# Kernel optimization log

Hardware: AMD Instinct MI355X
Metric: run time of the kernel (lower is better)

The kernel has to match this reference:

```python
import jax, jax.numpy as jnp
import numpy as np

L_RTN = 3  # complex taps produced by the RTN head (w_rtn3 out dim = 2*L_RTN)
EPS = 1e-12


def _to_complex(x):
    # (B, 2n) real interleaved [re0, im0, re1, im1, ...] -> (B, n) complex
    return x[:, 0::2] + 1j * x[:, 1::2]


def _to_real(xc):
    # (B, n) complex -> (B, 2n) real interleaved
    b, n = xc.shape
    return jnp.stack([xc.real, xc.imag], axis=-1).reshape(b, 2 * n)


def _complex_conv_taps(h_c, x_c):
    # per-sample causal complex FIR: out[t] = sum_l h[l] * x[t-l]
    # h_c: (B, L) complex, x_c: (B, n) complex
    n = x_c.shape[1]
    out = jnp.zeros_like(x_c)
    for l in range(h_c.shape[1]):  # L is tiny and static
        shifted = jnp.pad(x_c, ((0, 0), (l, 0)))[:, :n]
        out = out + h_c[:, l:l + 1] * shifted
    return out


def setup_inputs() -> dict:
    key = jax.random.key(0)
    ks = jax.random.split(key, 16)
    B, D_IN, H1, CH, H_RTN, H2, D_OUT = 8192, 512, 4096, 256, 1024, 4096, 512
    s = 0.02  # weight init scale
    x = jax.random.normal(ks[0], (B, D_IN), jnp.float32)
    w1 = s * jax.random.normal(ks[1], (H1, D_IN), jnp.float32)
    b1 = jnp.zeros((H1,), jnp.float32)
    w2 = s * jax.random.normal(ks[2], (CH, H1), jnp.float32)
    b2 = jnp.zeros((CH,), jnp.float32)
    w_rtn1 = s * jax.random.normal(ks[3], (H_RTN, CH), jnp.float32)
    b_rtn1 = jnp.zeros((H_RTN,), jnp.float32)
    w_rtn2 = s * jax.random.normal(ks[4], (H_RTN, H_RTN), jnp.float32)
    b_rtn2 = jnp.zeros((H_RTN,), jnp.float32)
    w_rtn3 = s * jax.random.normal(ks[5], (2 * L_RTN, H_RTN), jnp.float32)
    # bias so that RTN starts near identity tap [1, 0, 0, ...]
    b_rtn3 = jnp.zeros((2 * L_RTN,), jnp.float32).at[0].set(1.0)
    w3 = s * jax.random.normal(ks[6], (H2, CH), jnp.float32)
    b3 = jnp.zeros((H2,), jnp.float32)
    w4 = s * jax.random.normal(ks[7], (D_OUT, H2), jnp.float32)
    b4 = jnp.zeros((D_OUT,), jnp.float32)
    h = jax.random.normal(ks[8], (2,), jnp.float32)
    h = h / jnp.linalg.norm(h)  # unit-power single-tap fading channel
    noise = 0.1 * jax.random.normal(ks[9], (B, CH), jnp.float32)
    return {"x": x, "w1": w1, "b1": b1, "w2": w2, "b2": b2,
            "w_rtn1": w_rtn1, "b_rtn1": b_rtn1, "w_rtn2": w_rtn2,
            "b_rtn2": b_rtn2, "w_rtn3": w_rtn3, "b_rtn3": b_rtn3,
            "w3": w3, "b3": b3, "w4": w4, "b4": b4, "h": h, "noise": noise}


def reference(x, w1, b1, w2, b2, w_rtn1, b_rtn1, w_rtn2, b_rtn2,
              w_rtn3, b_rtn3, w3, b3, w4, b4, h, noise):
    # encoder (linear1 -> relu -> linear2)
    a = jax.nn.relu(x @ w1.T + b1)
    s = a @ w2.T + b2                      # (B, 2n) channel signal
    # power normalization: sqrt(2n) * sqrt(0.5) * s / ||s||
    scale = jnp.sqrt(s.shape[1] * 0.5)
    s = scale * s / jnp.linalg.norm(s, axis=1, keepdims=True)
    tx_c = _to_complex(s)                  # (B, n) transmitted symbols
    # single-tap complex channel
    h_c = h[0] + 1j * h[1]
    y = _to_real(h_c * tx_c) + noise       # add per-sample AWGN
    y_c = _to_complex(y)
    # LS channel estimate (1 tap): h_est = <y, x> / <x, x>
    num = jnp.sum(y_c * jnp.conj(tx_c), axis=1, keepdims=True)
    den = jnp.sum(jnp.abs(tx_c) ** 2, axis=1, keepdims=True)
    h_est = num / den                      # (B, 1)
    # zero-forcing signal estimate
    x_eq = y_c * jnp.conj(h_est) / (jnp.abs(h_est) ** 2 + EPS)
    xr = _to_real(x_eq)                    # (B, 2n)
    # RTN: predict inverse taps and apply per-sample complex conv
    g = jnp.tanh(xr @ w_rtn1.T + b_rtn1)
    g = jnp.tanh(g @ w_rtn2.T + b_rtn2)
    h_inv = g @ w_rtn3.T + b_rtn3          # (B, 2*L_RTN)
    h_inv_c = h_inv[:, 0::2] + 1j * h_inv[:, 1::2]
    xr = _to_real(_complex_conv_taps(h_inv_c, _to_complex(xr)))
    # decoder (linear3 -> relu -> linear4)
    out = jax.nn.relu(xr @ w3.T + b3)
    return out @ w4.T + b4
```

## Files before the change

### kernel.cpp

```cpp
#include <hip/hip_runtime.h>
#include <hip/hip_bf16.h>
#include <math.h>

using bf16 = __hip_bfloat16;
typedef __attribute__((ext_vector_type(8))) short short8;
typedef __attribute__((ext_vector_type(4))) float float4v;

template <typename T> __device__ inline T cvt_out(float v);
template <> __device__ inline float cvt_out<float>(float v) { return v; }
template <> __device__ inline bf16 cvt_out<bf16>(float v) { return __float2bfloat16(v); }

__device__ inline void gload_lds16(const bf16* g, bf16* l) {
    __builtin_amdgcn_global_load_lds(
        (const __attribute__((address_space(1))) void*)g,
        (__attribute__((address_space(3))) void*)l, 16, 0, 0);
}

struct CvtPack {
    const float* src[7];
    bf16* dst[7];
    int end[7];
};

__global__ __launch_bounds__(256) void cvt_all(CvtPack p) {
    int e = (blockIdx.x * 256 + threadIdx.x) * 4;
    int start = 0;
#pragma unroll
    for (int s = 0; s < 7; ++s) {
        if (e < p.end[s]) {
            int off = e - start;
            float4 v = *(const float4*)(p.src[s] + off);
            bf16* d = p.dst[s] + off;
            d[0] = __float2bfloat16(v.x);
            d[1] = __float2bfloat16(v.y);
            d[2] = __float2bfloat16(v.z);
            d[3] = __float2bfloat16(v.w);
            return;
        }
        start = p.end[s];
    }
}

__device__ inline float4 load4f(const float* p) { return *(const float4*)p; }
__device__ inline float4 load4f(const bf16* p) {
    ushort4 u = *(const ushort4*)p;
    float4 r;
    r.x = __uint_as_float((unsigned)u.x << 16);
    r.y = __uint_as_float((unsigned)u.y << 16);
    r.z = __uint_as_float((unsigned)u.z << 16);
    r.w = __uint_as_float((unsigned)u.w << 16);
    return r;
}
__device__ inline void store4(float* p, float4 v) { *(float4*)p = v; }
__device__ inline void store4(bf16* p, float4 v) {
    p[0] = __float2bfloat16(v.x); p[1] = __float2bfloat16(v.y);
    p[2] = __float2bfloat16(v.z); p[3] = __float2bfloat16(v.w);
}

template <int NK, int ACT, typename InT, typename OutT>
__global__ __launch_bounds__(256) void reduceK(const InT* __restrict__ p,
                                               const float* __restrict__ bias,
                                               OutT* __restrict__ out,
                                               size_t mn, int nmask, int total4) {
    int i = blockIdx.x * 256 + threadIdx.x;
    if (i < total4) {
        int idx = i * 4;
        float4 r = *(const float4*)(bias + (idx & nmask));
#pragma unroll
        for (int k = 0; k < NK; ++k) {
            float4 a = load4f(p + k * mn + idx);
            r.x += a.x; r.y += a.y; r.z += a.z; r.w += a.w;
        }
        if (ACT == 1) {
            r.x = fmaxf(r.x, 0.f); r.y = fmaxf(r.y, 0.f);
            r.z = fmaxf(r.z, 0.f); r.w = fmaxf(r.w, 0.f);
        } else if (ACT == 2) {
            r.x = tanhf(r.x); r.y = tanhf(r.y);
            r.z = tanhf(r.z); r.w = tanhf(r.w);
        }
        store4(out + idx, r);
    }
}

template <int ACT, typename OutT, bool PARTIAL>
__global__ __launch_bounds__(512, 2) void gemm_pipe(const bf16* __restrict__ A,
                                                    const bf16* __restrict__ W,
                                                    const float* __restrict__ bias,
                                                    OutT* __restrict__ C,
                                                    int M, int N, int K,
                                                    int nbn, int kcount) {
    __shared__ bf16 As[2][256 * 64];
    __shared__ bf16 Bs[2][256 * 64];

    const int bi = blockIdx.x;
    const int xcd = bi & 7, t = bi >> 3;
    const int bn = t % nbn;
    const int bm = xcd + 8 * (t / nbn);
    const int kbeg = PARTIAL ? blockIdx.y * kcount : 0;
    OutT* Cp = PARTIAL ? C + (size_t)blockIdx.y * M * N : C;

    const int tid = threadIdx.x;
    const int wave = tid >> 6, lane = tid & 63;
    const int wm = (wave >> 2) * 128, wn = (wave & 3) * 64;
    const int quad = lane >> 4, lrow = lane & 15;

    const bf16* Ab0 = A + (size_t)(bm * 256) * K + kbeg;
    const bf16* Wb0 = W + (size_t)(bn * 256) * K + kbeg;

    auto stage = [&](int kt, int bsel) {
        const int k0 = kt * 64;
#pragma unroll
        for (int tt = 0; tt < 4; ++tt) {
            int base = tt * 512 + wave * 64;
            int c = base + lane;
            int row = c >> 3, ch = c & 7;
            gload_lds16(Ab0 + (size_t)row * K + k0 + ((ch ^ (row & 7)) << 3),
                        &As[bsel][0] + base * 8);
        }
#pragma unroll
        for (int tt = 0; tt < 4; ++tt) {
            int base = tt * 512 + wave * 64;
            int c = base + lane;
            int row = c >> 3, ch = c & 7;
            gload_lds16(Wb0 + (size_t)row * K + k0 + ((ch ^ (row & 7)) << 3),
                        &Bs[bsel][0] + base * 8);
        }
    };

    float4v acc[8][4] = {};
    const int NT = kcount >> 6;

    stage(0, 0);
    if (NT > 1) {
        stage(1, 1);
        asm volatile("s_waitcnt vmcnt(8)" ::: "memory");
    } else {
        asm volatile("s_waitcnt vmcnt(0)" ::: "memory");
    }
    __builtin_amdgcn_s_barrier();

    const int swz = lrow & 7;
    for (int kt = 0; kt < NT; ++kt) {
        const bf16* Ap = &As[kt & 1][0];
        const bf16* Bp = &Bs[kt & 1][0];
        short8 af[2][8], bfr[2][4];
#pragma unroll
        for (int ks = 0; ks < 2; ++ks) {
            const int cswz = (((ks * 4 + quad) ^ swz) << 3);
#pragma unroll
            for (int i = 0; i < 8; ++i)
                af[ks][i] = *(const short8*)(Ap + (wm + i * 16 + lrow) * 64 + cswz);
#pragma unroll
            for (int j = 0; j < 4; ++j)
                bfr[ks][j] = *(const short8*)(Bp + (wn + j * 16 + lrow) * 64 + cswz);
        }
        asm volatile("s_waitcnt lgkmcnt(0)" ::: "memory");
        __builtin_amdgcn_s_barrier();
        if (kt + 2 < NT) stage(kt + 2, kt & 1);
        __builtin_amdgcn_s_setprio(1);
#pragma unroll
        for (int ks = 0; ks < 2; ++ks)
#pragma unroll
            for (int i = 0; i < 8; ++i)
#pragma unroll
                for (int j = 0; j < 4; ++j)
                    acc[i][j] = __builtin_amdgcn_mfma_f32_16x16x32_bf16(
                        af[ks][i], bfr[ks][j], acc[i][j], 0, 0, 0);
        __builtin_amdgcn_s_setprio(0);
        if (kt + 1 < NT) {
            if (kt + 2 < NT) asm volatile("s_waitcnt vmcnt(8)" ::: "memory");
            else             asm volatile("s_waitcnt vmcnt(0)" ::: "memory");
            __builtin_amdgcn_s_barrier();
        }
    }

#pragma unroll
    for (int i = 0; i < 8; ++i) {
        int m0 = bm * 256 + wm + i * 16 + quad * 4;
#pragma unroll
        for (int j = 0; j < 4; ++j) {
            int n = bn * 256 + wn + j * 16 + lrow;
            if constexpr (PARTIAL) {
#pragma unroll
                for (int r = 0; r < 4; ++r)
                    Cp[(size_t)(m0 + r) * N + n] = cvt_out<OutT>(acc[i][j][r]);
            } else {
                float bv = bias[n];
#pragma unroll
                for (int r = 0; r < 4; ++r) {
                    float v = acc[i][j][r] + bv;
                    if (ACT == 1) v = fmaxf(v, 0.f);
                    else if (ACT == 2) v = tanhf(v);
                    Cp[(size_t)(m0 + r) * N + n] = cvt_out<OutT>(v);
                }
            }
        }
    }
}

template <int ACT, typename OutT, int WMT, int WNT, int BKT, bool PARTIAL>
__global__ __launch_bounds__(256) void gemm_bt(const bf16* __restrict__ A,
                                               const bf16* __restrict__ W,
                                               const float* __restrict__ bias,
                                               OutT* __restrict__ C,
                                               int M, int N, int K,
                                               int nbn, int kcount) {
    constexpr int TBM = 32 * WMT;
    constexpr int TBN = 32 * WNT;
    constexpr int CPR = BKT / 8;
    constexpr int CA = TBM * CPR;
    constexpr int CB = TBN * CPR;

    __shared__ bf16 As[TBM * BKT];
    __shared__ bf16 Bs[TBN * BKT];

    const int bi = blockIdx.x;
    const int xcd = bi & 7, t = bi >> 3;
    const int bn = t % nbn;
    const int bm = xcd + 8 * (t / nbn);
    const int kbeg = PARTIAL ? blockIdx.y * kcount : 0;
    OutT* Cp = PARTIAL ? C + (size_t)blockIdx.y * M * N : C;

    const int tid = threadIdx.x;
    const int wave = tid >> 6, lane = tid & 63;
    const int wm = (wave >> 1) * (16 * WMT), wn = (wave & 1) * (16 * WNT);
    const int quad = lane >> 4, lrow = lane & 15;

    float4v acc[WMT][WNT] = {};
    const size_t arow = (size_t)(bm * TBM) * K;
    const size_t brow = (size_t)(bn * TBN) * K;

    for (int k0 = kbeg; k0 < kbeg + kcount; k0 += BKT) {
        __syncthreads();
#pragma unroll
        for (int tt = 0; tt < CA / 256; ++tt) {
            int base = tt * 256 + wave * 64;
            int c = base + lane;
            int row = c / CPR, col = (c % CPR) * 8;
            gload_lds16(A + arow + (size_t)row * K + k0 + col, As + base * 8);
        }
#pragma unroll
        for (int tt = 0; tt < CB / 256; ++tt) {
            int base = tt * 256 + wave * 64;
            int c = base + lane;
            int row = c / CPR, col = (c % CPR) * 8;
            gload_lds16(W + brow + (size_t)row * K + k0 + col, Bs + base * 8);
        }
        __syncthreads();
#pragma unroll
        for (int kk = 0; kk < BKT; kk += 32) {
            short8 af[WMT], bfr[WNT];
#pragma unroll
            for (int i = 0; i < WMT; ++i)
                af[i] = *(const short8*)(As + (wm + i * 16 + lrow) * BKT + kk + quad * 8);
#pragma unroll
            for (int j = 0; j < WNT; ++j)
                bfr[j] = *(const short8*)(Bs + (wn + j * 16 + lrow) * BKT + kk + quad * 8);
#pragma unroll
            for (int i = 0; i < WMT; ++i)
#pragma unroll
                for (int j = 0; j < WNT; ++j)
                    acc[i][j] = __builtin_amdgcn_mfma_f32_16x16x32_bf16(af[i], bfr[j], acc[i][j], 0, 0, 0);
        }
    }

#pragma unroll
    for (int i = 0; i < WMT; ++i) {
        int m0 = bm * TBM + wm + i * 16 + quad * 4;
#pragma unroll
        for (int j = 0; j < WNT; ++j) {
            int n = bn * TBN + wn + j * 16 + lrow;
            if constexpr (PARTIAL) {
#pragma unroll
                for (int r = 0; r < 4; ++r)
                    Cp[(size_t)(m0 + r) * N + n] = cvt_out<OutT>(acc[i][j][r]);
            } else {
                float bv = bias[n];
#pragma unroll
                for (int r = 0; r < 4; ++r) {
                    float v = acc[i][j][r] + bv;
                    if (ACT == 1) v = fmaxf(v, 0.f);
                    else if (ACT == 2) v = tanhf(v);
                    Cp[(size_t)(m0 + r) * N + n] = cvt_out<OutT>(v);
                }
            }
        }
    }
}

__global__ __launch_bounds__(64) void channel_kernel(const float* __restrict__ s,
                                                     const float* __restrict__ h,
                                                     const float* __restrict__ noise,
                                                     float* __restrict__ xr_f,
                                                     bf16* __restrict__ xr_b) {
    const int b = blockIdx.x, lane = threadIdx.x;
    const float* srow = s + (size_t)b * 256;

    float ss = 0.f;
#pragma unroll
    for (int t = 0; t < 4; ++t) {
        float v = srow[lane + 64 * t];
        ss += v * v;
    }
#pragma unroll
    for (int off = 32; off; off >>= 1) ss += __shfl_xor(ss, off);
    const float inv = sqrtf(128.0f) / sqrtf(ss);

    const float hre = h[0], him = h[1];

    float yre[2], yim[2];
    float nre = 0.f, nim = 0.f, den = 0.f;
#pragma unroll
    for (int t = 0; t < 2; ++t) {
        int c = lane + 64 * t;
        float tr = srow[2 * c] * inv, ti = srow[2 * c + 1] * inv;
        float yr = hre * tr - him * ti + noise[(size_t)b * 256 + 2 * c];
        float yi = hre * ti + him * tr + noise[(size_t)b * 256 + 2 * c + 1];
        yre[t] = yr; yim[t] = yi;
        nre += yr * tr + yi * ti;
        nim += yi * tr - yr * ti;
        den += tr * tr + ti * ti;
    }
#pragma unroll
    for (int off = 32; off; off >>= 1) {
        nre += __shfl_xor(nre, off);
        nim += __shfl_xor(nim, off);
        den += __shfl_xor(den, off);
    }
    const float her = nre / den, hei = nim / den;
    const float d2 = her * her + hei * hei + 1e-12f;

#pragma unroll
    for (int t = 0; t < 2; ++t) {
        int c = lane + 64 * t;
        float xre = (yre[t] * her + yim[t] * hei) / d2;
        float xim = (yim[t] * her - yre[t] * hei) / d2;
        xr_f[(size_t)b * 256 + 2 * c] = xre;
        xr_f[(size_t)b * 256 + 2 * c + 1] = xim;
        xr_b[(size_t)b * 256 + 2 * c] = __float2bfloat16(xre);
        xr_b[(size_t)b * 256 + 2 * c + 1] = __float2bfloat16(xim);
    }
}

__global__ __launch_bounds__(64) void rtn_taps_conv(const bf16* __restrict__ g2,
                                                    const float* __restrict__ wr3,
                                                    const float* __restrict__ br3,
                                                    const float* __restrict__ xr_f,
                                                    bf16* __restrict__ xr2) {
    const int b = blockIdx.x, lane = threadIdx.x;
    const bf16* grow = g2 + (size_t)b * 1024;

    float acc[6] = {0.f, 0.f, 0.f, 0.f, 0.f, 0.f};
#pragma unroll
    for (int t = 0; t < 16; ++t) {
        int k = lane + 64 * t;
        float gv = __bfloat162float(grow[k]);
#pragma unroll
        for (int j = 0; j < 6; ++j) acc[j] += gv * wr3[j * 1024 + k];
    }
#pragma unroll
    for (int j = 0; j < 6; ++j)
#pragma unroll
        for (int off = 32; off; off >>= 1) acc[j] += __shfl_xor(acc[j], off);

    float tre[3], tim[3];
#pragma unroll
    for (int l = 0; l < 3; ++l) {
        tre[l] = acc[2 * l] + br3[2 * l];
        tim[l] = acc[2 * l + 1] + br3[2 * l + 1];
    }

    const float* xrow = xr_f + (size_t)b * 256;
#pragma unroll
    for (int t = 0; t < 2; ++t) {
        int c = lane + 64 * t;
        float ore = 0.f, oim = 0.f;
#pragma unroll
        for (int l = 0; l < 3; ++l) {
            int cc = c - l;
            if (cc >= 0) {
                float xre = xrow[2 * cc], xim = xrow[2 * cc + 1];
                ore += tre[l] * xre - tim[l] * xim;
                oim += tre[l] * xim + tim[l] * xre;
            }
        }
        xr2[(size_t)b * 256 + 2 * c] = __float2bfloat16(ore);
        xr2[(size_t)b * 256 + 2 * c + 1] = __float2bfloat16(oim);
    }
}

extern "C" void kernel_launch(void* const* d_in, const int* in_sizes, int n_in,
                              void* d_out, int out_size, void* d_ws, size_t ws_size,
                              hipStream_t stream) {
    constexpr int B = 8192, D_IN = 512, H1 = 4096, CH = 256, HR = 1024, H2 = 4096, DOUT = 512;

    const float* x   = (const float*)d_in[0];
    const float* w1  = (const float*)d_in[1];
    const float* b1  = (const float*)d_in[2];
    const float* w2  = (const float*)d_in[3];
    const float* b2  = (const float*)d_in[4];
    const float* wr1 = (const float*)d_in[5];
    const float* br1 = (const float*)d_in[6];
    const float* wr2 = (const float*)d_in[7];
    const float* br2 = (const float*)d_in[8];
    const float* wr3 = (const float*)d_in[9];
    const float* br3 = (const float*)d_in[10];
    const float* w3  = (const float*)d_in[11];
    const float* b3  = (const float*)d_in[12];
    const float* w4  = (const float*)d_in[13];
    const float* b4  = (const float*)d_in[14];
    const float* h   = (const float*)d_in[15];
    const float* noise = (const float*)d_in[16];

    char* ws = (char*)d_ws;
    bf16*  a    = (bf16*)(ws + 0);
    float* sF   = (float*)(ws + 0);
    bf16*  g1   = (bf16*)(ws + 0);
    bf16*  g2   = (bf16*)(ws + 16777216);
    bf16*  tbuf = (bf16*)(ws + 0);
    bf16*  w1B  = (bf16*)(ws + 67108864);
    bf16*  w2B  = (bf16*)(ws + 71303168);
    bf16*  wr1B = (bf16*)(ws + 73400320);
    bf16*  wr2B = (bf16*)(ws + 73924608);
    bf16*  w3B  = (bf16*)(ws + 76021760);
    bf16*  w4B  = (bf16*)(ws + 78118912);
    bf16*  xB   = (bf16*)(ws + 82313216);
    bf16*  g2P  = (bf16*)(ws + 82313216);
    float* xrF  = (float*)(ws + 99090432);
    bf16*  xrB  = (bf16*)(ws + 107479040);
    bf16*  xr2  = (bf16*)(ws + 111673344);
    bf16*  g6P  = (bf16*)(ws + 82313216);

    dim3 blk(256);

    CvtPack p;
    const float* srcs[7] = {x, w1, w2, wr1, wr2, w3, w4};
    bf16* dsts[7] = {xB, w1B, w2B, wr1B, wr2B, w3B, w4B};
    int ns[7] = {B * D_IN, H1 * D_IN, CH * H1, HR * CH, HR * HR, H2 * CH, DOUT * H2};
    int cum = 0;
    for (int i = 0; i < 7; ++i) { p.src[i] = srcs[i]; p.dst[i] = dsts[i]; cum += ns[i]; p.end[i] = cum; }
    cvt_all<<<(cum / 4 + 255) / 256, blk, 0, stream>>>(p);

    gemm_pipe<1, bf16, false><<<dim3(32 * 16), dim3(512), 0, stream>>>(
        xB, w1B, b1, a, B, H1, D_IN, 16, D_IN);
    gemm_pipe<0, bf16, true><<<dim3(32, 8), dim3(512), 0, stream>>>(
        a, w2B, nullptr, g2P, B, CH, H1, 1, H1 / 8);
    reduceK<8, 0, bf16, float><<<(B * CH / 4 + 255) / 256, blk, 0, stream>>>(
        g2P, b2, sF, (size_t)B * CH, CH - 1, B * CH / 4);
    channel_kernel<<<B, 64, 0, stream>>>(sF, h, noise, xrF, xrB);
    gemm_bt<2, bf16, 4, 2, 64, false><<<64 * 16, blk, 0, stream>>>(
        xrB, wr1B, br1, g1, B, HR, CH, 16, CH);
    gemm_bt<2, bf16, 4, 2, 64, false><<<64 * 16, blk, 0, stream>>>(
        g1, wr2B, br2, g2, B, HR, HR, 16, HR);
    rtn_taps_conv<<<B, 64, 0, stream>>>(g2, wr3, br3, xrF, xr2);
    gemm_pipe<1, bf16, false><<<dim3(32 * 16), dim3(512), 0, stream>>>(
        xr2, w3B, b3, tbuf, B, H2, CH, 16, CH);
    gemm_pipe<0, bf16, true><<<dim3(32 * 2, 4), dim3(512), 0, stream>>>(
        tbuf, w4B, nullptr, g6P, B, DOUT, H2, 2, H2 / 4);
    reduceK<4, 0, bf16, float><<<(B * DOUT / 4 + 255) / 256, blk, 0, stream>>>(
        g6P, b4, (float*)d_out, (size_t)B * DOUT, DOUT - 1, B * DOUT / 4);
}
```

Before: 342.0 us.

## Restructure 256x256 GEMM into quadrant-interleaved 8-wave pipeline and split-K RTN layer

```diff
diff --git a/kernel.cpp b/kernel.cpp
--- a/kernel.cpp
+++ b/kernel.cpp
@@ -83,14 +83,14 @@
 }
 
 template <int ACT, typename OutT, bool PARTIAL>
-__global__ __launch_bounds__(512, 2) void gemm_pipe(const bf16* __restrict__ A,
-                                                    const bf16* __restrict__ W,
-                                                    const float* __restrict__ bias,
-                                                    OutT* __restrict__ C,
-                                                    int M, int N, int K,
-                                                    int nbn, int kcount) {
-    __shared__ bf16 As[2][256 * 64];
-    __shared__ bf16 Bs[2][256 * 64];
+__global__ __launch_bounds__(512, 2) void gemm_pipe8(const bf16* __restrict__ A,
+                                                     const bf16* __restrict__ W,
+                                                     const float* __restrict__ bias,
+                                                     OutT* __restrict__ C,
+                                                     int M, int N, int K,
+                                                     int nbn, int kcount) {
+    __shared__ bf16 As[2][2][128 * 64];
+    __shared__ bf16 Bs[2][2][128 * 64];
 
     const int bi = blockIdx.x;
     const int xcd = bi & 7, t = bi >> 3;
@@ -101,101 +101,132 @@
 
     const int tid = threadIdx.x;
     const int wave = tid >> 6, lane = tid & 63;
-    const int wm = (wave >> 2) * 128, wn = (wave & 3) * 64;
+    const int mwave = (wave >> 2) * 64, nwave = (wave & 3) * 32;
     const int quad = lane >> 4, lrow = lane & 15;
-
-    const bf16* Ab0 = A + (size_t)(bm * 256) * K + kbeg;
-    const bf16* Wb0 = W + (size_t)(bn * 256) * K + kbeg;
-
-    auto stage = [&](int kt, int bsel) {
-        const int k0 = kt * 64;
-#pragma unroll
-        for (int tt = 0; tt < 4; ++tt) {
+    const int swz = lrow & 7;
+
+    const bf16* Ab = A + (size_t)(bm * 256) * K + kbeg;
+    const bf16* Wb = W + (size_t)(bn * 256) * K + kbeg;
+    const int NT = kcount >> 6;
+
+    auto stA = [&](int tl, int h) {
+        if (tl >= NT) return;
+#pragma unroll
+        for (int tt = 0; tt < 2; ++tt) {
             int base = tt * 512 + wave * 64;
             int c = base + lane;
             int row = c >> 3, ch = c & 7;
-            gload_lds16(Ab0 + (size_t)row * K + k0 + ((ch ^ (row & 7)) << 3),
-                        &As[bsel][0] + base * 8);
-        }
-#pragma unroll
-        for (int tt = 0; tt < 4; ++tt) {
+            gload_lds16(Ab + (size_t)(h * 128 + row) * K + tl * 64 + ((ch ^ (row & 7)) << 3),
+                        &As[tl & 1][h][0] + base * 8);
+        }
+    };
+    auto stB = [&](int tl, int h) {
+        if (tl >= NT) return;
+#pragma unroll
+        for (int tt = 0; tt < 2; ++tt) {
             int base = tt * 512 + wave * 64;
             int c = base + lane;
             int row = c >> 3, ch = c & 7;
-            gload_lds16(Wb0 + (size_t)row * K + k0 + ((ch ^ (row & 7)) << 3),
-                        &Bs[bsel][0] + base * 8);
+            gload_lds16(Wb + (size_t)(h * 128 + row) * K + tl * 64 + ((ch ^ (row & 7)) << 3),
+                        &Bs[tl & 1][h][0] + base * 8);
         }
     };
 
-    float4v acc[8][4] = {};
-    const int NT = kcount >> 6;
-
-    stage(0, 0);
-    if (NT > 1) {
-        stage(1, 1);
-        asm volatile("s_waitcnt vmcnt(8)" ::: "memory");
-    } else {
-        asm volatile("s_waitcnt vmcnt(0)" ::: "memory");
-    }
+    float4v acc[2][2][4][2] = {};
+    short8 af[4][2], bfv[2][2];
+
+#define LDA8(BUF, MH)                                                         \
+    { const bf16* pA = &As[BUF][MH][0];                                       \
+      _Pragma("unroll") for (int i = 0; i < 4; ++i)                           \
+        _Pragma("unroll") for (int ks = 0; ks < 2; ++ks)                      \
+          af[i][ks] = *(const short8*)(pA + (mwave + i * 16 + lrow) * 64 +    \
+                                       (((ks * 4 + quad) ^ swz) << 3)); }
+#define LDB8(BUF, NH)                                                         \
+    { const bf16* pB = &Bs[BUF][NH][0];                                       \
+      _Pragma("unroll") for (int j = 0; j < 2; ++j)                           \
+        _Pragma("unroll") for (int ks = 0; ks < 2; ++ks)                      \
+          bfv[j][ks] = *(const short8*)(pB + (nwave + j * 16 + lrow) * 64 +   \
+                                        (((ks * 4 + quad) ^ swz) << 3)); }
+#define MM8(MH, NH)                                                           \
+    { _Pragma("unroll") for (int ks = 0; ks < 2; ++ks)                        \
+        _Pragma("unroll") for (int i = 0; i < 4; ++i)                         \
+          _Pragma("unroll") for (int j = 0; j < 2; ++j)                       \
+            acc[MH][NH][i][j] = __builtin_amdgcn_mfma_f32_16x16x32_bf16(      \
+                af[i][ks], bfv[j][ks], acc[MH][NH][i][j], 0, 0, 0); }
+#define SYNC_IN                                                               \
+    __builtin_amdgcn_s_barrier();                                             \
+    asm volatile("s_waitcnt lgkmcnt(0)" ::: "memory");                        \
+    __builtin_amdgcn_sched_barrier(0);                                        \
+    __builtin_amdgcn_s_setprio(1);
+#define SYNC_OUT                                                              \
+    __builtin_amdgcn_s_setprio(0);                                            \
     __builtin_amdgcn_s_barrier();
 
-    const int swz = lrow & 7;
-    for (int kt = 0; kt < NT; ++kt) {
-        const bf16* Ap = &As[kt & 1][0];
-        const bf16* Bp = &Bs[kt & 1][0];
-        short8 af[2][8], bfr[2][4];
-#pragma unroll
-        for (int ks = 0; ks < 2; ++ks) {
-            const int cswz = (((ks * 4 + quad) ^ swz) << 3);
-#pragma unroll
-            for (int i = 0; i < 8; ++i)
-                af[ks][i] = *(const short8*)(Ap + (wm + i * 16 + lrow) * 64 + cswz);
-#pragma unroll
-            for (int j = 0; j < 4; ++j)
-                bfr[ks][j] = *(const short8*)(Bp + (wn + j * 16 + lrow) * 64 + cswz);
-        }
-        asm volatile("s_waitcnt lgkmcnt(0)" ::: "memory");
+    stA(0, 0); stB(0, 0); stA(0, 1); stB(0, 1);
+    stA(1, 0); stB(1, 1);
+    if (NT > 1) asm volatile("s_waitcnt vmcnt(4)" ::: "memory");
+    else        asm volatile("s_waitcnt vmcnt(0)" ::: "memory");
+    __builtin_amdgcn_s_barrier();
+
+    for (int T = 0; T < NT; T += 2) {
+        LDA8(0, 0); LDB8(0, 0); stA(T + 1, 1);
+        SYNC_IN; MM8(0, 0); SYNC_OUT;
+        LDB8(0, 1); stB(T + 1, 0);
+        SYNC_IN; MM8(0, 1); SYNC_OUT;
+        LDA8(0, 1); stA(T + 2, 0);
+        SYNC_IN; MM8(1, 1); SYNC_OUT;
+        LDB8(0, 0); stB(T + 2, 1);
+        SYNC_IN; MM8(1, 0);
+        __builtin_amdgcn_s_setprio(0);
+        if (T + 2 < NT) asm volatile("s_waitcnt vmcnt(4)" ::: "memory");
+        else            asm volatile("s_waitcnt vmcnt(0)" ::: "memory");
         __builtin_amdgcn_s_barrier();
-        if (kt + 2 < NT) stage(kt + 2, kt & 1);
-        __builtin_amdgcn_s_setprio(1);
-#pragma unroll
-        for (int ks = 0; ks < 2; ++ks)
-#pragma unroll
-            for (int i = 0; i < 8; ++i)
-#pragma unroll
-                for (int j = 0; j < 4; ++j)
-                    acc[i][j] = __builtin_amdgcn_mfma_f32_16x16x32_bf16(
-                        af[ks][i], bfr[ks][j], acc[i][j], 0, 0, 0);
+        LDA8(1, 0); LDB8(1, 0); stA(T + 2, 1);
+        SYNC_IN; MM8(0, 0); SYNC_OUT;
+        LDB8(1, 1); stB(T + 2, 0);
+        SYNC_IN; MM8(0, 1); SYNC_OUT;
+        LDA8(1, 1); stA(T + 3, 0);
+        SYNC_IN; MM8(1, 1); SYNC_OUT;
+        LDB8(1, 0); stB(T + 3, 1);
+        SYNC_IN; MM8(1, 0);
         __builtin_amdgcn_s_setprio(0);
-        if (kt + 1 < NT) {
-            if (kt + 2 < NT) asm volatile("s_waitcnt vmcnt(8)" ::: "memory");
-            else             asm volatile("s_waitcnt vmcnt(0)" ::: "memory");
+        if (T + 2 < NT) {
+            asm volatile("s_waitcnt vmcnt(4)" ::: "memory");
             __builtin_amdgcn_s_barrier();
         }
     }
-
-#pragma unroll
-    for (int i = 0; i < 8; ++i) {
-        int m0 = bm * 256 + wm + i * 16 + quad * 4;
-#pragma unroll
-        for (int j = 0; j < 4; ++j) {
-            int n = bn * 256 + wn + j * 16 + lrow;
-            if constexpr (PARTIAL) {
-#pragma unroll
-                for (int r = 0; r < 4; ++r)
-                    Cp[(size_t)(m0 + r) * N + n] = cvt_out<OutT>(acc[i][j][r]);
-            } else {
-                float bv = bias[n];
-#pragma unroll
-                for (int r = 0; r < 4; ++r) {
-                    float v = acc[i][j][r] + bv;
-                    if (ACT == 1) v = fmaxf(v, 0.f);
-                    else if (ACT == 2) v = tanhf(v);
-                    Cp[(size_t)(m0 + r) * N + n] = cvt_out<OutT>(v);
+#undef LDA8
+#undef LDB8
+#undef MM8
+#undef SYNC_IN
+#undef SYNC_OUT
+
+#pragma unroll
+    for (int mh = 0; mh < 2; ++mh)
+#pragma unroll
+        for (int i = 0; i < 4; ++i) {
+            int m0 = bm * 256 + mh * 128 + mwave + i * 16 + quad * 4;
+#pragma unroll
+            for (int nh = 0; nh < 2; ++nh)
+#pragma unroll
+                for (int j = 0; j < 2; ++j) {
+                    int n = bn * 256 + nh * 128 + nwave + j * 16 + lrow;
+                    if constexpr (PARTIAL) {
+#pragma unroll
+                        for (int r = 0; r < 4; ++r)
+                            Cp[(size_t)(m0 + r) * N + n] = cvt_out<OutT>(acc[mh][nh][i][j][r]);
+                    } else {
+                        float bv = bias[n];
+#pragma unroll
+                        for (int r = 0; r < 4; ++r) {
+                            float v = acc[mh][nh][i][j][r] + bv;
+                            if (ACT == 1) v = fmaxf(v, 0.f);
+                            else if (ACT == 2) v = tanhf(v);
+                            Cp[(size_t)(m0 + r) * N + n] = cvt_out<OutT>(v);
+                        }
+                    }
                 }
-            }
-        }
-    }
+        }
 }
 
 template <int ACT, typename OutT, int WMT, int WNT, int BKT, bool PARTIAL>
@@ -417,6 +448,7 @@
     float* sF   = (float*)(ws + 0);
     bf16*  g1   = (bf16*)(ws + 0);
     bf16*  g2   = (bf16*)(ws + 16777216);
+    bf16*  g4P  = (bf16*)(ws + 33554432);
     bf16*  tbuf = (bf16*)(ws + 0);
     bf16*  w1B  = (bf16*)(ws + 67108864);
     bf16*  w2B  = (bf16*)(ws + 71303168);
@@ -441,21 +473,23 @@
     for (int i = 0; i < 7; ++i) { p.src[i] = srcs[i]; p.dst[i] = dsts[i]; cum += ns[i]; p.end[i] = cum; }
     cvt_all<<<(cum / 4 + 255) / 256, blk, 0, stream>>>(p);
 
-    gemm_pipe<1, bf16, false><<<dim3(32 * 16), dim3(512), 0, stream>>>(
+    gemm_pipe8<1, bf16, false><<<dim3(32 * 16), dim3(512), 0, stream>>>(
         xB, w1B, b1, a, B, H1, D_IN, 16, D_IN);
-    gemm_pipe<0, bf16, true><<<dim3(32, 8), dim3(512), 0, stream>>>(
+    gemm_pipe8<0, bf16, true><<<dim3(32, 8), dim3(512), 0, stream>>>(
         a, w2B, nullptr, g2P, B, CH, H1, 1, H1 / 8);
     reduceK<8, 0, bf16, float><<<(B * CH / 4 + 255) / 256, blk, 0, stream>>>(
         g2P, b2, sF, (size_t)B * CH, CH - 1, B * CH / 4);
     channel_kernel<<<B, 64, 0, stream>>>(sF, h, noise, xrF, xrB);
     gemm_bt<2, bf16, 4, 2, 64, false><<<64 * 16, blk, 0, stream>>>(
         xrB, wr1B, br1, g1, B, HR, CH, 16, CH);
-    gemm_bt<2, bf16, 4, 2, 64, false><<<64 * 16, blk, 0, stream>>>(
-        g1, wr2B, br2, g2, B, HR, HR, 16, HR);
+    gemm_pipe8<0, bf16, true><<<dim3(32 * 4, 2), dim3(512), 0, stream>>>(
+        g1, wr2B, nullptr, g4P, B, HR, HR, 4, HR / 2);
+    reduceK<2, 2, bf16, bf16><<<(B * HR / 4 + 255) / 256, blk, 0, stream>>>(
+        g4P, br2, g2, (size_t)B * HR, HR - 1, B * HR / 4);
     rtn_taps_conv<<<B, 64, 0, stream>>>(g2, wr3, br3, xrF, xr2);
-    gemm_pipe<1, bf16, false><<<dim3(32 * 16), dim3(512), 0, stream>>>(
+    gemm_pipe8<1, bf16, false><<<dim3(32 * 16), dim3(512), 0, stream>>>(
         xr2, w3B, b3, tbuf, B, H2, CH, 16, CH);
-    gemm_pipe<0, bf16, true><<<dim3(32 * 2, 4), dim3(512), 0, stream>>>(
+    gemm_pipe8<0, bf16, true><<<dim3(32 * 2, 4), dim3(512), 0, stream>>>(
         tbuf, w4B, nullptr, g6P, B, DOUT, H2, 2, H2 / 4);
     reduceK<4, 0, bf16, float><<<(B * DOUT / 4 + 255) / 256, blk, 0, stream>>>(
         g6P, b4, (float*)d_out, (size_t)B * DOUT, DOUT - 1, B * DOUT / 4);
```

Measured after the change: 342.7 us. Within noise of the previous version (+0.2%).
